# Kernel tuning notes

Hardware: AMD Instinct MI355X
Metric: run time of the kernel (lower is better)

The kernel has to match this reference:

```python
import jax, jax.numpy as jnp
import numpy as np

N = 100000      # nodes
E = 1600000     # edges (avg degree 16)
IN = 128        # in_channels
OUT = 64        # out_channels
HID = 2 * OUT   # hidden = 2*out_channels


def setup_inputs() -> dict:
    key = jax.random.key(0)
    ks = jax.random.split(key, 9)
    x = jax.random.normal(ks[0], (N, IN), jnp.float32)
    edge_index = jax.random.randint(ks[1], (2, E), 0, N, jnp.int32)
    init_dist = jax.random.normal(ks[2], (N, OUT), jnp.float32)
    # GCNConv weights (glorot-ish scale) and biases
    W1 = jax.random.normal(ks[3], (IN, HID), jnp.float32) * (1.0 / np.sqrt(IN))
    b1 = jnp.zeros((HID,), jnp.float32)
    Wmu = jax.random.normal(ks[4], (HID, OUT), jnp.float32) * (1.0 / np.sqrt(HID))
    bmu = jnp.zeros((OUT,), jnp.float32)
    Wls = jax.random.normal(ks[5], (HID, OUT), jnp.float32) * (1.0 / np.sqrt(HID))
    bls = jnp.zeros((OUT,), jnp.float32)
    return {"x": x, "edge_index": edge_index, "init_dist": init_dist,
            "W1": W1, "b1": b1, "Wmu": Wmu, "bmu": bmu, "Wls": Wls, "bls": bls}


def _gcn(h, src, dst, norm, W, b, n):
    # dense transform, then normalized scatter-add aggregation over edges
    h = h @ W                               # [N, F]
    msg = h[src] * norm[:, None]            # gather + scale  [E', F]
    out = jax.ops.segment_sum(msg, dst, num_segments=n)
    return out + b


def reference(x, edge_index, init_dist, W1, b1, Wmu, bmu, Wls, bls):
    n = x.shape[0]
    # add self-loops (PyG GCNConv default)
    loops = jnp.arange(n, dtype=edge_index.dtype)
    src = jnp.concatenate([edge_index[0], loops])
    dst = jnp.concatenate([edge_index[1], loops])
    # symmetric normalization: deg over A+I, norm_e = d_src^-1/2 * d_dst^-1/2
    deg = jax.ops.segment_sum(jnp.ones_like(dst, dtype=x.dtype), dst, num_segments=n)
    dinv = jax.lax.rsqrt(jnp.maximum(deg, 1.0))  # deg >= 1 thanks to self-loops
    norm = dinv[src] * dinv[dst]

    h = _gcn(x, src, dst, norm, W1, b1, n)       # conv1 (no activation in source)
    mu = _gcn(h, src, dst, norm, Wmu, bmu, n)
    logstd = _gcn(h, src, dst, norm, Wls, bls, n)
    # reparametrize: mu + init_dist * exp(logstd)
    return mu + init_dist * jnp.exp(logstd)
```

## Files before the change

kernel.cpp:

```cpp
#include <hip/hip_runtime.h>
#include <math.h>

#define NN 100000
#define NE 1600000
#define SLOTS 48
#define NODES_PER_BUCKET 12500
#define SEGS 256
#define QUADS (NE / 4)
#define QPS ((QUADS + SEGS - 1) / SEGS)

__device__ __forceinline__ float bf2f(unsigned int u) {
    union { unsigned int u; float f; } c; c.u = u << 16; return c.f;
}
__device__ __forceinline__ unsigned short f2bf(float f) {
    union { float f; unsigned int u; } c; c.f = f;
    unsigned int x = c.u;
    return (unsigned short)((x + 0x7fffu + ((x >> 16) & 1u)) >> 16);
}

typedef __attribute__((ext_vector_type(8))) short short8;
typedef __attribute__((ext_vector_type(4))) float float4v;

__global__ __launch_bounds__(256) void k_count_fill_b(const int* __restrict__ ei,
        int* __restrict__ cnt, int* __restrict__ csr48) {
    int bucket = blockIdx.x & 7;
    int seg = blockIdx.x >> 3;
    int lo = bucket * NODES_PER_BUCKET, hi = lo + NODES_PER_BUCKET;
    int q1 = min((seg + 1) * QPS, QUADS);
    for (int q = seg * QPS + threadIdx.x; q < q1; q += 256) {
        int e0 = q * 4;
        int4 s = *(const int4*)(ei + e0);
        int4 d = *(const int4*)(ei + NE + e0);
        int r;
        if (d.x >= lo && d.x < hi) { r = atomicAdd(&cnt[d.x], 1); if (r < SLOTS) csr48[d.x * SLOTS + r] = s.x; }
        if (d.y >= lo && d.y < hi) { r = atomicAdd(&cnt[d.y], 1); if (r < SLOTS) csr48[d.y * SLOTS + r] = s.y; }
        if (d.z >= lo && d.z < hi) { r = atomicAdd(&cnt[d.z], 1); if (r < SLOTS) csr48[d.z * SLOTS + r] = s.z; }
        if (d.w >= lo && d.w < hi) { r = atomicAdd(&cnt[d.w], 1); if (r < SLOTS) csr48[d.w * SLOTS + r] = s.w; }
    }
}

__global__ __launch_bounds__(256) void k_wprep(const float* __restrict__ W1,
        const float* __restrict__ Wmu, const float* __restrict__ Wls,
        const float* __restrict__ b1,
        unsigned short* __restrict__ W2c, float* __restrict__ bw, int* __restrict__ cnt) {
    int idx = blockIdx.x * 256 + threadIdx.x;
    if (idx < 16384) {
        int k = idx >> 7, n = idx & 127;
        const float* Wx = (n < 64) ? (Wmu + n) : (Wls + (n - 64));
        float s = 0.f;
#pragma unroll 8
        for (int m = 0; m < 128; ++m) s += W1[k * 128 + m] * Wx[(size_t)m * 64];
        W2c[n * 128 + k] = f2bf(s);
    } else if (idx < 16512) {
        int n = idx - 16384;
        const float* Wx = (n < 64) ? (Wmu + n) : (Wls + (n - 64));
        float s = 0.f;
        for (int m = 0; m < 128; ++m) s += b1[m] * Wx[(size_t)m * 64];
        bw[n] = s;
    } else {
        for (int i = idx - 16512; i < NN; i += 24576 - 16512) cnt[i] = 0;
    }
}

__global__ __launch_bounds__(256) void k_prescale(const float* __restrict__ x,
        const int* __restrict__ cnt, float* __restrict__ dinv, unsigned short* __restrict__ xs) {
    int i = blockIdx.x * 256 + threadIdx.x;
    if (i >= NN * 32) return;
    int node = i >> 5, c = (i & 31) << 2;
    float d = rsqrtf((float)(cnt[node] + 1));
    if ((i & 31) == 0) dinv[node] = d;
    float4 v = *(const float4*)(x + (size_t)node * 128 + c);
    uint2 st;
    st.x = ((unsigned int)f2bf(d * v.y) << 16) | f2bf(d * v.x);
    st.y = ((unsigned int)f2bf(d * v.w) << 16) | f2bf(d * v.z);
    *(uint2*)(xs + (size_t)node * 128 + c) = st;
}

__global__ __launch_bounds__(256) void k_gather1(
    const unsigned short* __restrict__ tab, const int* __restrict__ cnt,
    const int* __restrict__ csr48, const float* __restrict__ dinv,
    unsigned short* __restrict__ yout, float* __restrict__ avec) {
    int node = blockIdx.x * 4 + (threadIdx.x >> 6);
    int lane = threadIdx.x & 63;
    int q = lane >> 4, l16 = lane & 15;
    float a[8] = {0.f, 0.f, 0.f, 0.f, 0.f, 0.f, 0.f, 0.f};
    float asum = 0.f;
    if (q == 0) {
        uint4 p = *(const uint4*)(tab + (size_t)node * 128 + l16 * 8);
        a[0] = bf2f(p.x & 0xffffu); a[1] = bf2f(p.x >> 16);
        a[2] = bf2f(p.y & 0xffffu); a[3] = bf2f(p.y >> 16);
        a[4] = bf2f(p.z & 0xffffu); a[5] = bf2f(p.z >> 16);
        a[6] = bf2f(p.w & 0xffffu); a[7] = bf2f(p.w >> 16);
    }
    int deg = __builtin_amdgcn_readfirstlane(cnt[node]);
    if (deg > SLOTS) deg = SLOTS;
    int base = node * SLOTS;
    int t = q;
    while (t + 4 < deg) {
        int s0 = csr48[base + t];
        int s1 = csr48[base + t + 4];
        uint4 r0 = *(const uint4*)(tab + (size_t)s0 * 128 + l16 * 8);
        uint4 r1 = *(const uint4*)(tab + (size_t)s1 * 128 + l16 * 8);
        asum += dinv[s0] + dinv[s1];
        a[0] += bf2f(r0.x & 0xffffu) + bf2f(r1.x & 0xffffu);
        a[1] += bf2f(r0.x >> 16)     + bf2f(r1.x >> 16);
        a[2] += bf2f(r0.y & 0xffffu) + bf2f(r1.y & 0xffffu);
        a[3] += bf2f(r0.y >> 16)     + bf2f(r1.y >> 16);
        a[4] += bf2f(r0.z & 0xffffu) + bf2f(r1.z & 0xffffu);
        a[5] += bf2f(r0.z >> 16)     + bf2f(r1.z >> 16);
        a[6] += bf2f(r0.w & 0xffffu) + bf2f(r1.w & 0xffffu);
        a[7] += bf2f(r0.w >> 16)     + bf2f(r1.w >> 16);
        t += 8;
    }
    while (t < deg) {
        int s = csr48[base + t];
        uint4 r = *(const uint4*)(tab + (size_t)s * 128 + l16 * 8);
        asum += dinv[s];
        a[0] += bf2f(r.x & 0xffffu); a[1] += bf2f(r.x >> 16);
        a[2] += bf2f(r.y & 0xffffu); a[3] += bf2f(r.y >> 16);
        a[4] += bf2f(r.z & 0xffffu); a[5] += bf2f(r.z >> 16);
        a[6] += bf2f(r.w & 0xffffu); a[7] += bf2f(r.w >> 16);
        t += 4;
    }
#pragma unroll
    for (int j = 0; j < 8; ++j) {
        a[j] += __shfl_xor(a[j], 16);
        a[j] += __shfl_xor(a[j], 32);
    }
    asum += __shfl_xor(asum, 16);
    asum += __shfl_xor(asum, 32);
    if (q == 0) {
        float di = dinv[node];
        float d2 = di * di;
        uint4 st;
        st.x = ((unsigned int)f2bf(a[1] * d2) << 16) | f2bf(a[0] * d2);
        st.y = ((unsigned int)f2bf(a[3] * d2) << 16) | f2bf(a[2] * d2);
        st.z = ((unsigned int)f2bf(a[5] * d2) << 16) | f2bf(a[4] * d2);
        st.w = ((unsigned int)f2bf(a[7] * d2) << 16) | f2bf(a[6] * d2);
        *(uint4*)(yout + (size_t)node * 128 + l16 * 8) = st;
        if (l16 == 0) avec[node] = di * (asum + di);
    }
}

__global__ __launch_bounds__(256) void k_gather2(
    const unsigned short* __restrict__ tab, const int* __restrict__ cnt,
    const int* __restrict__ csr48, const float* __restrict__ dinv,
    unsigned short* __restrict__ yout) {
    int node = blockIdx.x * 4 + (threadIdx.x >> 6);
    int lane = threadIdx.x & 63;
    int q = lane >> 4, l16 = lane & 15;
    float a[8] = {0.f, 0.f, 0.f, 0.f, 0.f, 0.f, 0.f, 0.f};
    if (q == 0) {
        uint4 p = *(const uint4*)(tab + (size_t)node * 128 + l16 * 8);
        a[0] = bf2f(p.x & 0xffffu); a[1] = bf2f(p.x >> 16);
        a[2] = bf2f(p.y & 0xffffu); a[3] = bf2f(p.y >> 16);
        a[4] = bf2f(p.z & 0xffffu); a[5] = bf2f(p.z >> 16);
        a[6] = bf2f(p.w & 0xffffu); a[7] = bf2f(p.w >> 16);
    }
    int deg = __builtin_amdgcn_readfirstlane(cnt[node]);
    if (deg > SLOTS) deg = SLOTS;
    int base = node * SLOTS;
    int t = q;
    while (t + 4 < deg) {
        int s0 = csr48[base + t];
        int s1 = csr48[base + t + 4];
        uint4 r0 = *(const uint4*)(tab + (size_t)s0 * 128 + l16 * 8);
        uint4 r1 = *(const uint4*)(tab + (size_t)s1 * 128 + l16 * 8);
        a[0] += bf2f(r0.x & 0xffffu) + bf2f(r1.x & 0xffffu);
        a[1] += bf2f(r0.x >> 16)     + bf2f(r1.x >> 16);
        a[2] += bf2f(r0.y & 0xffffu) + bf2f(r1.y & 0xffffu);
        a[3] += bf2f(r0.y >> 16)     + bf2f(r1.y >> 16);
        a[4] += bf2f(r0.z & 0xffffu) + bf2f(r1.z & 0xffffu);
        a[5] += bf2f(r0.z >> 16)     + bf2f(r1.z >> 16);
        a[6] += bf2f(r0.w & 0xffffu) + bf2f(r1.w & 0xffffu);
        a[7] += bf2f(r0.w >> 16)     + bf2f(r1.w >> 16);
        t += 8;
    }
    while (t < deg) {
        int s = csr48[base + t];
        uint4 r = *(const uint4*)(tab + (size_t)s * 128 + l16 * 8);
        a[0] += bf2f(r.x & 0xffffu); a[1] += bf2f(r.x >> 16);
        a[2] += bf2f(r.y & 0xffffu); a[3] += bf2f(r.y >> 16);
        a[4] += bf2f(r.z & 0xffffu); a[5] += bf2f(r.z >> 16);
        a[6] += bf2f(r.w & 0xffffu); a[7] += bf2f(r.w >> 16);
        t += 4;
    }
#pragma unroll
    for (int j = 0; j < 8; ++j) {
        a[j] += __shfl_xor(a[j], 16);
        a[j] += __shfl_xor(a[j], 32);
    }
    if (q == 0) {
        float di = dinv[node];
        uint4 st;
        st.x = ((unsigned int)f2bf(a[1] * di) << 16) | f2bf(a[0] * di);
        st.y = ((unsigned int)f2bf(a[3] * di) << 16) | f2bf(a[2] * di);
        st.z = ((unsigned int)f2bf(a[5] * di) << 16) | f2bf(a[4] * di);
        st.w = ((unsigned int)f2bf(a[7] * di) << 16) | f2bf(a[6] * di);
        *(uint4*)(yout + (size_t)node * 128 + l16 * 8) = st;
    }
}

__global__ __launch_bounds__(256) void k_gemmC(
    const unsigned short* __restrict__ g2,
    const unsigned short* __restrict__ Bt,
    const float* __restrict__ bw,
    const float* __restrict__ avec,
    const float* __restrict__ bmu,
    const float* __restrict__ bls,
    const float* __restrict__ init,
    float* __restrict__ outp,
    int nrows) {
    __shared__ __align__(16) unsigned short As[64 * 136];
    int tid = threadIdx.x;
    int r0 = blockIdx.x * 64;
    for (int c = tid; c < 1024; c += 256) {
        int row = c >> 4, kc = (c & 15) << 3;
        int gr = r0 + row;
        short8 v = {0, 0, 0, 0, 0, 0, 0, 0};
        if (gr < nrows) v = *(const short8*)(g2 + (size_t)gr * 128 + kc);
        *(short8*)(As + row * 136 + kc) = v;
    }
    __syncthreads();
    int lane = tid & 63, wave = tid >> 6;
    int quad = lane >> 4, l16 = lane & 15;
    int cm = wave * 16 + l16;
    int cl = 64 + cm;
    float4v acc[4][2];
#pragma unroll
    for (int rt = 0; rt < 4; ++rt) {
        float4v z = {0.f, 0.f, 0.f, 0.f};
        acc[rt][0] = z; acc[rt][1] = z;
    }
#pragma unroll
    for (int ks = 0; ks < 4; ++ks) {
        short8 b0 = *(const short8*)(Bt + (size_t)cm * 128 + ks * 32 + quad * 8);
        short8 b1 = *(const short8*)(Bt + (size_t)cl * 128 + ks * 32 + quad * 8);
        short8 af[4];
#pragma unroll
        for (int rt = 0; rt < 4; ++rt)
            af[rt] = *(const short8*)(As + (rt * 16 + l16) * 136 + ks * 32 + quad * 8);
#pragma unroll
        for (int rt = 0; rt < 4; ++rt) {
            acc[rt][0] = __builtin_amdgcn_mfma_f32_16x16x32_bf16(af[rt], b0, acc[rt][0], 0, 0, 0);
            acc[rt][1] = __builtin_amdgcn_mfma_f32_16x16x32_bf16(af[rt], b1, acc[rt][1], 0, 0, 0);
        }
    }
    float bc_mu = bmu[cm], bc_ls = bls[cm];
    float bwm = bw[cm], bwl = bw[cl];
#pragma unroll
    for (int rt = 0; rt < 4; ++rt)
#pragma unroll
        for (int reg = 0; reg < 4; ++reg) {
            int gr = r0 + rt * 16 + quad * 4 + reg;
            if (gr < nrows) {
                float av = avec[gr];
                float mu = acc[rt][0][reg] + av * bwm + bc_mu;
                float ls = acc[rt][1][reg] + av * bwl + bc_ls;
                float idv = init[(size_t)gr * 64 + cm];
                outp[(size_t)gr * 64 + cm] = mu + idv * expf(ls);
            }
        }
}

extern "C" void kernel_launch(void* const* d_in, const int* in_sizes, int n_in,
                              void* d_out, int out_size, void* d_ws, size_t ws_size,
                              hipStream_t stream) {
    const float* x   = (const float*)d_in[0];
    const int*   ei  = (const int*)d_in[1];
    const float* ind = (const float*)d_in[2];
    const float* W1  = (const float*)d_in[3];
    const float* b1  = (const float*)d_in[4];
    const float* Wmu = (const float*)d_in[5];
    const float* bmu = (const float*)d_in[6];
    const float* Wls = (const float*)d_in[7];
    const float* bls = (const float*)d_in[8];
    float* outp = (float*)d_out;

    char* w = (char*)d_ws;
    auto carve = [&](size_t bytes) -> char* {
        char* p = w; w += (bytes + 255) & ~(size_t)255; return p;
    };
    int*   cnt  = (int*)carve((size_t)NN * 4);
    float* dinv = (float*)carve((size_t)NN * 4);
    float* avec = (float*)carve((size_t)NN * 4);
    float* bw   = (float*)carve(128 * 4);
    unsigned short* W2c = (unsigned short*)carve(128 * 128 * 2);
    unsigned short* xs  = (unsigned short*)carve((size_t)NN * 128 * 2);
    unsigned short* t1  = (unsigned short*)carve((size_t)NN * 128 * 2);
    int* csr = (int*)carve((size_t)NN * SLOTS * 4);

    k_wprep<<<96, 256, 0, stream>>>(W1, Wmu, Wls, b1, W2c, bw, cnt);
    k_count_fill_b<<<8 * SEGS, 256, 0, stream>>>(ei, cnt, csr);
    k_prescale<<<(NN * 32 + 255) / 256, 256, 0, stream>>>(x, cnt, dinv, xs);
    k_gather1<<<NN / 4, 256, 0, stream>>>(xs, cnt, csr, dinv, t1, avec);
    k_gather2<<<NN / 4, 256, 0, stream>>>(t1, cnt, csr, dinv, xs);
    k_gemmC<<<(NN + 63) / 64, 256, 0, stream>>>(xs, W2c, bw, avec, bmu, bls, ind, outp, NN);
}
```

Baseline: 376.2 us.

## Fuse CSR build, x cast and weight prep into one front kernel

Merges edge counting/CSR fill, the x-to-bf16 cast, and the weight premultiply into a single kernel launch, replacing the old cnt zeroing with a memset. The x cast no longer depends on degrees, so it can run concurrently with the atomics. The dinv array is dropped: gather1 and gather2 recompute rsqrt(cnt+1) per node and per neighbour, and gather1 applies the source-side scaling inside its loop. The aim is fewer launches and serialization points, paid for with extra random cnt reads and rsqrt work in gather1.

Result: faster. 356.0 us (-5.4%).

```diff
diff --git a/kernel.cpp b/kernel.cpp
--- a/kernel.cpp
+++ b/kernel.cpp
@@ -5,9 +5,13 @@
 #define NE 1600000
 #define SLOTS 48
 #define NODES_PER_BUCKET 12500
-#define SEGS 256
 #define QUADS (NE / 4)
-#define QPS ((QUADS + SEGS - 1) / SEGS)
+#define CSEG 128
+#define QPS2 ((QUADS + CSEG - 1) / CSEG)
+#define XCAST_T (NN * 32)
+#define PREP_T (XCAST_T + 16384 + 128)
+#define PREP_B ((PREP_T + 255) / 256)
+#define FRONT_B (1024 + PREP_B)
 
 __device__ __forceinline__ float bf2f(unsigned int u) {
     union { unsigned int u; float f; } c; c.u = u << 16; return c.f;
@@ -21,105 +25,103 @@
 typedef __attribute__((ext_vector_type(8))) short short8;
 typedef __attribute__((ext_vector_type(4))) float float4v;
 
-__global__ __launch_bounds__(256) void k_count_fill_b(const int* __restrict__ ei,
-        int* __restrict__ cnt, int* __restrict__ csr48) {
-    int bucket = blockIdx.x & 7;
-    int seg = blockIdx.x >> 3;
-    int lo = bucket * NODES_PER_BUCKET, hi = lo + NODES_PER_BUCKET;
-    int q1 = min((seg + 1) * QPS, QUADS);
-    for (int q = seg * QPS + threadIdx.x; q < q1; q += 256) {
-        int e0 = q * 4;
-        int4 s = *(const int4*)(ei + e0);
-        int4 d = *(const int4*)(ei + NE + e0);
-        int r;
-        if (d.x >= lo && d.x < hi) { r = atomicAdd(&cnt[d.x], 1); if (r < SLOTS) csr48[d.x * SLOTS + r] = s.x; }
-        if (d.y >= lo && d.y < hi) { r = atomicAdd(&cnt[d.y], 1); if (r < SLOTS) csr48[d.y * SLOTS + r] = s.y; }
-        if (d.z >= lo && d.z < hi) { r = atomicAdd(&cnt[d.z], 1); if (r < SLOTS) csr48[d.z * SLOTS + r] = s.z; }
-        if (d.w >= lo && d.w < hi) { r = atomicAdd(&cnt[d.w], 1); if (r < SLOTS) csr48[d.w * SLOTS + r] = s.w; }
-    }
-}
-
-__global__ __launch_bounds__(256) void k_wprep(const float* __restrict__ W1,
-        const float* __restrict__ Wmu, const float* __restrict__ Wls,
-        const float* __restrict__ b1,
-        unsigned short* __restrict__ W2c, float* __restrict__ bw, int* __restrict__ cnt) {
-    int idx = blockIdx.x * 256 + threadIdx.x;
-    if (idx < 16384) {
-        int k = idx >> 7, n = idx & 127;
-        const float* Wx = (n < 64) ? (Wmu + n) : (Wls + (n - 64));
-        float s = 0.f;
+__global__ __launch_bounds__(256) void k_front(const int* __restrict__ ei,
+        int* __restrict__ cnt, int* __restrict__ csr48,
+        const float* __restrict__ x, unsigned short* __restrict__ xq,
+        const float* __restrict__ W1, const float* __restrict__ Wmu,
+        const float* __restrict__ Wls, const float* __restrict__ b1,
+        unsigned short* __restrict__ W2c, float* __restrict__ bw) {
+    int b = blockIdx.x;
+    if (b < 1024) {
+        int bucket = b & 7;
+        int seg = b >> 3;
+        int lo = bucket * NODES_PER_BUCKET, hi = lo + NODES_PER_BUCKET;
+        int q1 = min((seg + 1) * QPS2, QUADS);
+        for (int q = seg * QPS2 + (int)threadIdx.x; q < q1; q += 256) {
+            int e0 = q * 4;
+            int4 s = *(const int4*)(ei + e0);
+            int4 d = *(const int4*)(ei + NE + e0);
+            int r;
+            if (d.x >= lo && d.x < hi) { r = atomicAdd(&cnt[d.x], 1); if (r < SLOTS) csr48[d.x * SLOTS + r] = s.x; }
+            if (d.y >= lo && d.y < hi) { r = atomicAdd(&cnt[d.y], 1); if (r < SLOTS) csr48[d.y * SLOTS + r] = s.y; }
+            if (d.z >= lo && d.z < hi) { r = atomicAdd(&cnt[d.z], 1); if (r < SLOTS) csr48[d.z * SLOTS + r] = s.z; }
+            if (d.w >= lo && d.w < hi) { r = atomicAdd(&cnt[d.w], 1); if (r < SLOTS) csr48[d.w * SLOTS + r] = s.w; }
+        }
+    } else {
+        int idx = (b - 1024) * 256 + (int)threadIdx.x;
+        if (idx < XCAST_T) {
+            int node = idx >> 5, c = (idx & 31) << 2;
+            float4 v = *(const float4*)(x + (size_t)node * 128 + c);
+            uint2 st;
+            st.x = ((unsigned int)f2bf(v.y) << 16) | f2bf(v.x);
+            st.y = ((unsigned int)f2bf(v.w) << 16) | f2bf(v.z);
+            *(uint2*)(xq + (size_t)node * 128 + c) = st;
+        } else if (idx < XCAST_T + 16384) {
+            int j = idx - XCAST_T;
+            int k = j >> 7, n = j & 127;
+            const float* Wx = (n < 64) ? (Wmu + n) : (Wls + (n - 64));
+            float s = 0.f;
 #pragma unroll 8
-        for (int m = 0; m < 128; ++m) s += W1[k * 128 + m] * Wx[(size_t)m * 64];
-        W2c[n * 128 + k] = f2bf(s);
-    } else if (idx < 16512) {
-        int n = idx - 16384;
-        const float* Wx = (n < 64) ? (Wmu + n) : (Wls + (n - 64));
-        float s = 0.f;
-        for (int m = 0; m < 128; ++m) s += b1[m] * Wx[(size_t)m * 64];
-        bw[n] = s;
-    } else {
-        for (int i = idx - 16512; i < NN; i += 24576 - 16512) cnt[i] = 0;
-    }
-}
-
-__global__ __launch_bounds__(256) void k_prescale(const float* __restrict__ x,
-        const int* __restrict__ cnt, float* __restrict__ dinv, unsigned short* __restrict__ xs) {
-    int i = blockIdx.x * 256 + threadIdx.x;
-    if (i >= NN * 32) return;
-    int node = i >> 5, c = (i & 31) << 2;
-    float d = rsqrtf((float)(cnt[node] + 1));
-    if ((i & 31) == 0) dinv[node] = d;
-    float4 v = *(const float4*)(x + (size_t)node * 128 + c);
-    uint2 st;
-    st.x = ((unsigned int)f2bf(d * v.y) << 16) | f2bf(d * v.x);
-    st.y = ((unsigned int)f2bf(d * v.w) << 16) | f2bf(d * v.z);
-    *(uint2*)(xs + (size_t)node * 128 + c) = st;
+            for (int m = 0; m < 128; ++m) s += W1[k * 128 + m] * Wx[(size_t)m * 64];
+            W2c[n * 128 + k] = f2bf(s);
+        } else if (idx < PREP_T) {
+            int n = idx - XCAST_T - 16384;
+            const float* Wx = (n < 64) ? (Wmu + n) : (Wls + (n - 64));
+            float s = 0.f;
+            for (int m = 0; m < 128; ++m) s += b1[m] * Wx[(size_t)m * 64];
+            bw[n] = s;
+        }
+    }
 }
 
 __global__ __launch_bounds__(256) void k_gather1(
     const unsigned short* __restrict__ tab, const int* __restrict__ cnt,
-    const int* __restrict__ csr48, const float* __restrict__ dinv,
+    const int* __restrict__ csr48,
     unsigned short* __restrict__ yout, float* __restrict__ avec) {
     int node = blockIdx.x * 4 + (threadIdx.x >> 6);
     int lane = threadIdx.x & 63;
     int q = lane >> 4, l16 = lane & 15;
+    int deg = __builtin_amdgcn_readfirstlane(cnt[node]);
+    float dn = rsqrtf((float)(deg + 1));
+    if (deg > SLOTS) deg = SLOTS;
     float a[8] = {0.f, 0.f, 0.f, 0.f, 0.f, 0.f, 0.f, 0.f};
     float asum = 0.f;
     if (q == 0) {
         uint4 p = *(const uint4*)(tab + (size_t)node * 128 + l16 * 8);
-        a[0] = bf2f(p.x & 0xffffu); a[1] = bf2f(p.x >> 16);
-        a[2] = bf2f(p.y & 0xffffu); a[3] = bf2f(p.y >> 16);
-        a[4] = bf2f(p.z & 0xffffu); a[5] = bf2f(p.z >> 16);
-        a[6] = bf2f(p.w & 0xffffu); a[7] = bf2f(p.w >> 16);
-    }
-    int deg = __builtin_amdgcn_readfirstlane(cnt[node]);
-    if (deg > SLOTS) deg = SLOTS;
+        a[0] = dn * bf2f(p.x & 0xffffu); a[1] = dn * bf2f(p.x >> 16);
+        a[2] = dn * bf2f(p.y & 0xffffu); a[3] = dn * bf2f(p.y >> 16);
+        a[4] = dn * bf2f(p.z & 0xffffu); a[5] = dn * bf2f(p.z >> 16);
+        a[6] = dn * bf2f(p.w & 0xffffu); a[7] = dn * bf2f(p.w >> 16);
+    }
     int base = node * SLOTS;
     int t = q;
     while (t + 4 < deg) {
         int s0 = csr48[base + t];
         int s1 = csr48[base + t + 4];
+        float d0 = rsqrtf((float)(cnt[s0] + 1));
+        float d1 = rsqrtf((float)(cnt[s1] + 1));
         uint4 r0 = *(const uint4*)(tab + (size_t)s0 * 128 + l16 * 8);
         uint4 r1 = *(const uint4*)(tab + (size_t)s1 * 128 + l16 * 8);
-        asum += dinv[s0] + dinv[s1];
-        a[0] += bf2f(r0.x & 0xffffu) + bf2f(r1.x & 0xffffu);
-        a[1] += bf2f(r0.x >> 16)     + bf2f(r1.x >> 16);
-        a[2] += bf2f(r0.y & 0xffffu) + bf2f(r1.y & 0xffffu);
-        a[3] += bf2f(r0.y >> 16)     + bf2f(r1.y >> 16);
-        a[4] += bf2f(r0.z & 0xffffu) + bf2f(r1.z & 0xffffu);
-        a[5] += bf2f(r0.z >> 16)     + bf2f(r1.z >> 16);
-        a[6] += bf2f(r0.w & 0xffffu) + bf2f(r1.w & 0xffffu);
-        a[7] += bf2f(r0.w >> 16)     + bf2f(r1.w >> 16);
+        asum += d0 + d1;
+        a[0] += d0 * bf2f(r0.x & 0xffffu) + d1 * bf2f(r1.x & 0xffffu);
+        a[1] += d0 * bf2f(r0.x >> 16)     + d1 * bf2f(r1.x >> 16);
+        a[2] += d0 * bf2f(r0.y & 0xffffu) + d1 * bf2f(r1.y & 0xffffu);
+        a[3] += d0 * bf2f(r0.y >> 16)     + d1 * bf2f(r1.y >> 16);
+        a[4] += d0 * bf2f(r0.z & 0xffffu) + d1 * bf2f(r1.z & 0xffffu);
+        a[5] += d0 * bf2f(r0.z >> 16)     + d1 * bf2f(r1.z >> 16);
+        a[6] += d0 * bf2f(r0.w & 0xffffu) + d1 * bf2f(r1.w & 0xffffu);
+        a[7] += d0 * bf2f(r0.w >> 16)     + d1 * bf2f(r1.w >> 16);
         t += 8;
     }
     while (t < deg) {
         int s = csr48[base + t];
+        float ds = rsqrtf((float)(cnt[s] + 1));
         uint4 r = *(const uint4*)(tab + (size_t)s * 128 + l16 * 8);
-        asum += dinv[s];
-        a[0] += bf2f(r.x & 0xffffu); a[1] += bf2f(r.x >> 16);
-        a[2] += bf2f(r.y & 0xffffu); a[3] += bf2f(r.y >> 16);
-        a[4] += bf2f(r.z & 0xffffu); a[5] += bf2f(r.z >> 16);
-        a[6] += bf2f(r.w & 0xffffu); a[7] += bf2f(r.w >> 16);
+        asum += ds;
+        a[0] += ds * bf2f(r.x & 0xffffu); a[1] += ds * bf2f(r.x >> 16);
+        a[2] += ds * bf2f(r.y & 0xffffu); a[3] += ds * bf2f(r.y >> 16);
+        a[4] += ds * bf2f(r.z & 0xffffu); a[5] += ds * bf2f(r.z >> 16);
+        a[6] += ds * bf2f(r.w & 0xffffu); a[7] += ds * bf2f(r.w >> 16);
         t += 4;
     }
 #pragma unroll
@@ -130,25 +132,26 @@
     asum += __shfl_xor(asum, 16);
     asum += __shfl_xor(asum, 32);
     if (q == 0) {
-        float di = dinv[node];
-        float d2 = di * di;
+        float d2 = dn * dn;
         uint4 st;
         st.x = ((unsigned int)f2bf(a[1] * d2) << 16) | f2bf(a[0] * d2);
         st.y = ((unsigned int)f2bf(a[3] * d2) << 16) | f2bf(a[2] * d2);
         st.z = ((unsigned int)f2bf(a[5] * d2) << 16) | f2bf(a[4] * d2);
         st.w = ((unsigned int)f2bf(a[7] * d2) << 16) | f2bf(a[6] * d2);
         *(uint4*)(yout + (size_t)node * 128 + l16 * 8) = st;
-        if (l16 == 0) avec[node] = di * (asum + di);
+        if (l16 == 0) avec[node] = dn * (asum + dn);
     }
 }
 
 __global__ __launch_bounds__(256) void k_gather2(
     const unsigned short* __restrict__ tab, const int* __restrict__ cnt,
-    const int* __restrict__ csr48, const float* __restrict__ dinv,
-    unsigned short* __restrict__ yout) {
+    const int* __restrict__ csr48, unsigned short* __restrict__ yout) {
     int node = blockIdx.x * 4 + (threadIdx.x >> 6);
     int lane = threadIdx.x & 63;
     int q = lane >> 4, l16 = lane & 15;
+    int deg = __builtin_amdgcn_readfirstlane(cnt[node]);
+    float dn = rsqrtf((float)(deg + 1));
+    if (deg > SLOTS) deg = SLOTS;
     float a[8] = {0.f, 0.f, 0.f, 0.f, 0.f, 0.f, 0.f, 0.f};
     if (q == 0) {
         uint4 p = *(const uint4*)(tab + (size_t)node * 128 + l16 * 8);
@@ -157,8 +160,6 @@
         a[4] = bf2f(p.z & 0xffffu); a[5] = bf2f(p.z >> 16);
         a[6] = bf2f(p.w & 0xffffu); a[7] = bf2f(p.w >> 16);
     }
-    int deg = __builtin_amdgcn_readfirstlane(cnt[node]);
-    if (deg > SLOTS) deg = SLOTS;
     int base = node * SLOTS;
     int t = q;
     while (t + 4 < deg) {
@@ -191,12 +192,11 @@
         a[j] += __shfl_xor(a[j], 32);
     }
     if (q == 0) {
-        float di = dinv[node];
         uint4 st;
-        st.x = ((unsigned int)f2bf(a[1] * di) << 16) | f2bf(a[0] * di);
-        st.y = ((unsigned int)f2bf(a[3] * di) << 16) | f2bf(a[2] * di);
-        st.z = ((unsigned int)f2bf(a[5] * di) << 16) | f2bf(a[4] * di);
-        st.w = ((unsigned int)f2bf(a[7] * di) << 16) | f2bf(a[6] * di);
+        st.x = ((unsigned int)f2bf(a[1] * dn) << 16) | f2bf(a[0] * dn);
+        st.y = ((unsigned int)f2bf(a[3] * dn) << 16) | f2bf(a[2] * dn);
+        st.z = ((unsigned int)f2bf(a[5] * dn) << 16) | f2bf(a[4] * dn);
+        st.w = ((unsigned int)f2bf(a[7] * dn) << 16) | f2bf(a[6] * dn);
         *(uint4*)(yout + (size_t)node * 128 + l16 * 8) = st;
     }
 }
@@ -282,7 +282,6 @@
         char* p = w; w += (bytes + 255) & ~(size_t)255; return p;
     };
     int*   cnt  = (int*)carve((size_t)NN * 4);
-    float* dinv = (float*)carve((size_t)NN * 4);
     float* avec = (float*)carve((size_t)NN * 4);
     float* bw   = (float*)carve(128 * 4);
     unsigned short* W2c = (unsigned short*)carve(128 * 128 * 2);
@@ -290,10 +289,9 @@
     unsigned short* t1  = (unsigned short*)carve((size_t)NN * 128 * 2);
     int* csr = (int*)carve((size_t)NN * SLOTS * 4);
 
-    k_wprep<<<96, 256, 0, stream>>>(W1, Wmu, Wls, b1, W2c, bw, cnt);
-    k_count_fill_b<<<8 * SEGS, 256, 0, stream>>>(ei, cnt, csr);
-    k_prescale<<<(NN * 32 + 255) / 256, 256, 0, stream>>>(x, cnt, dinv, xs);
-    k_gather1<<<NN / 4, 256, 0, stream>>>(xs, cnt, csr, dinv, t1, avec);
-    k_gather2<<<NN / 4, 256, 0, stream>>>(t1, cnt, csr, dinv, xs);
+    hipMemsetAsync(cnt, 0, (size_t)NN * 4, stream);
+    k_front<<<FRONT_B, 256, 0, stream>>>(ei, cnt, csr, x, xs, W1, Wmu, Wls, b1, W2c, bw);
+    k_gather1<<<NN / 4, 256, 0, stream>>>(xs, cnt, csr, t1, avec);
+    k_gather2<<<NN / 4, 256, 0, stream>>>(t1, cnt, csr, xs);
     k_gemmC<<<(NN + 63) / 64, 256, 0, stream>>>(xs, W2c, bw, avec, bmu, bls, ind, outp, NN);
 }
```
